# Kernel optimization log

Hardware: AMD Instinct MI355X
Metric: run time of the kernel (lower is better)

## Reference

```python
import jax, jax.numpy as jnp
import numpy as np

B, C, N, V, W = 2, 4, 224, 7, 256
EMB, H = 256, 4
TOKEN_DIM = C * N           # 896
HF = int(C * 2.66)          # 10 (GDFN hidden features)
EPS_LN = 1e-6


def _dwconv3(x, w):
    # depthwise 3x3, padding=1; x:[B,Ch,Hh,Ww], w:[Ch,1,3,3]
    return jax.lax.conv_general_dilated(
        x, w, window_strides=(1, 1), padding='SAME',
        feature_group_count=x.shape[1],
        dimension_numbers=('NCHW', 'OIHW', 'NCHW'))


def _layernorm_c(x, g, b):
    # LayerNorm over channel dim (NCHW), eps=1e-6
    m = jnp.mean(x, axis=1, keepdims=True)
    v = jnp.mean((x - m) ** 2, axis=1, keepdims=True)
    return (x - m) / jnp.sqrt(v + EPS_LN) * g[None, :, None, None] + b[None, :, None, None]


def setup_inputs() -> dict:
    key = jax.random.key(0)
    ks = jax.random.split(key, 12)
    s = 0.02
    return {
        'buffer':     jax.random.normal(ks[0], (B, C, N, V, W), jnp.float32),
        'w_in':       jax.random.normal(ks[1], (EMB, TOKEN_DIM), jnp.float32) * s,
        'temperature': jnp.ones((1, H, 1, 1), jnp.float32),
        'ln1_g':      jnp.ones((EMB,), jnp.float32),
        'ln1_b':      jnp.zeros((EMB,), jnp.float32),
        'w_qkv':      jax.random.normal(ks[2], (3 * EMB, EMB), jnp.float32) * s,
        'w_qkv_dw':   jax.random.normal(ks[3], (3 * EMB, 1, 3, 3), jnp.float32) * s,
        'w_proj':     jax.random.normal(ks[4], (TOKEN_DIM, EMB), jnp.float32) * s,
        'w_attca':    jax.random.normal(ks[5], (2 * H, H), jnp.float32) * s,
        'ln2_g':      jnp.ones((C,), jnp.float32),
        'ln2_b':      jnp.zeros((C,), jnp.float32),
        'w_pin':      jax.random.normal(ks[6], (2 * HF, C), jnp.float32) * s,
        'w_dw':       jax.random.normal(ks[7], (2 * HF, 1, 3, 3), jnp.float32) * s,
        'w_pout':     jax.random.normal(ks[8], (C, HF), jnp.float32) * s,
    }


def reference(buffer, w_in, temperature, ln1_g, ln1_b, w_qkv, w_qkv_dw,
              w_proj, w_attca, ln2_g, ln2_b, w_pin, w_dw, w_pout):
    S = V * W
    d = EMB // H
    # b c n v w -> b (v w) (c n)
    x_tok = buffer.transpose(0, 3, 4, 1, 2).reshape(B, S, C * N)
    # b c n v w -> (b n) c v w
    x_res = buffer.transpose(0, 2, 1, 3, 4).reshape(B * N, C, V, W)

    x_tok = jnp.einsum('bsk,ek->bse', x_tok, w_in)                  # linear_in
    x = x_tok.reshape(B, V, W, EMB).transpose(0, 3, 1, 2)           # b emb v w
    x_norm = _layernorm_c(x, ln1_g, ln1_b)

    qkv = jnp.einsum('bchw,oc->bohw', x_norm, w_qkv)                # 1x1 conv
    qkv = _dwconv3(qkv, w_qkv_dw)
    q, k, v_ = jnp.split(qkv, 3, axis=1)

    def heads(t):  # b (h d) v w -> b h (v w) d
        return t.reshape(B, H, d, S).transpose(0, 1, 3, 2)
    q, k, v_ = heads(q), heads(k), heads(v_)

    # F.normalize(dim=-1), eps=1e-12
    q = q / jnp.maximum(jnp.linalg.norm(q, axis=-1, keepdims=True), 1e-12)
    k = k / jnp.maximum(jnp.linalg.norm(k, axis=-1, keepdims=True), 1e-12)

    attn_logits = jnp.einsum('bhid,bhjd->bhij', q, k) * temperature
    attn0 = jax.nn.softmax(attn_logits, axis=-1)
    attn1 = jnp.maximum(attn_logits, 0.0) ** 2
    attn1 = jax.nn.gelu(attn1, approximate=False) * attn1
    x_att = jnp.einsum('bhij,oh->boij', attn1, w_attca)             # 1x1 conv over heads
    scale, shift = jnp.split(x_att, 2, axis=1)
    attn = attn0 * (1.0 + scale) + shift

    out = jnp.einsum('bhij,bhjd->bhid', attn, v_)
    out = out.transpose(0, 1, 3, 2).reshape(B, EMB, V, W)           # b (h d) v w
    out = jnp.einsum('bchw,oc->bohw', out, w_proj)                  # proj to token_dim
    out = out.reshape(B, C, N, V, W).transpose(0, 2, 1, 3, 4).reshape(B * N, C, V, W)

    x2 = x_res + out
    epi = _layernorm_c(x2, ln2_g, ln2_b)
    # GDFN
    h_ = jnp.einsum('bchw,oc->bohw', epi, w_pin)
    h_ = _dwconv3(h_, w_dw)
    h1, h2 = jnp.split(h_, 2, axis=1)
    h_ = jax.nn.gelu(h1, approximate=False) * h2
    epi = jnp.einsum('bchw,oc->bohw', h_, w_pout)
    epi = x2 + epi

    return epi.reshape(B, N, C, V, W).transpose(0, 2, 1, 3, 4)      # b c n v w
```

## Files before the change

### kernel.cpp

```cpp
#include <hip/hip_runtime.h>
#include <math.h>

#define B_ 2
#define C_ 4
#define N_ 224
#define V_ 7
#define W_ 256
#define S_ 1792
#define EMB_ 256
#define H_ 4
#define D_ 64
#define TOK_ 896
#define HF_ 10
#define JC_ 8
#define JRANGE_ (S_ / JC_)
#define JSTEPS_ (JRANGE_ / 32)

typedef __attribute__((ext_vector_type(8))) short short8;
typedef __attribute__((ext_vector_type(4))) float f32x4;

#define MFMA16(a, b, c) __builtin_amdgcn_mfma_f32_16x16x32_bf16(a, b, c, 0, 0, 0)

__device__ inline short f2bf(float f) {
    union { float f; unsigned u; } x; x.f = f;
    unsigned u = x.u;
    unsigned r = (u + 0x7fffu + ((u >> 16) & 1u)) >> 16;
    return (short)r;
}
__device__ inline float bf2f(short s) {
    union { unsigned u; float f; } x;
    x.u = ((unsigned)(unsigned short)s) << 16;
    return x.f;
}

__global__ __launch_bounds__(256) void gemm64_kernel(
    const float* __restrict__ A, const float* __restrict__ Bact, float* __restrict__ Cm,
    int M, int N, int K, long b_bs, long c_bs,
    const float* __restrict__ mu, const float* __restrict__ ri,
    const float* __restrict__ lg, const float* __restrict__ lb)
{
    const int bz = blockIdx.z;
    Bact += (long)bz * b_bs;
    Cm   += (long)bz * c_bs;
    const int m0 = blockIdx.y * 64, n0 = blockIdx.x * 64;
    __shared__ __align__(16) short As[64 * 32];
    __shared__ __align__(16) short Bs[64 * 32];
    const int t = threadIdx.x;
    const int lane = t & 63, wave = t >> 6;
    const int wr = wave >> 1, wc = wave & 1;
    const int col = lane & 15, grp = lane >> 4;
    const int s_row = t >> 2, s_ch = t & 3;
    const int bn = t & 63, bkc = t >> 6;
    float mun = 0.f, rin = 1.f;
    if (mu) { mun = mu[(long)bz * N + n0 + bn]; rin = ri[(long)bz * N + n0 + bn]; }
    f32x4 acc[2][2];
    #pragma unroll
    for (int i = 0; i < 2; ++i)
        #pragma unroll
        for (int j = 0; j < 2; ++j) acc[i][j] = (f32x4){0.f, 0.f, 0.f, 0.f};
    for (int k0 = 0; k0 < K; k0 += 32) {
        const float* ap = &A[(long)(m0 + s_row) * K + k0 + s_ch * 8];
        f32x4 a0 = *(const f32x4*)ap;
        f32x4 a1 = *(const f32x4*)(ap + 4);
        short8 av;
        av[0] = f2bf(a0[0]); av[1] = f2bf(a0[1]); av[2] = f2bf(a0[2]); av[3] = f2bf(a0[3]);
        av[4] = f2bf(a1[0]); av[5] = f2bf(a1[1]); av[6] = f2bf(a1[2]); av[7] = f2bf(a1[3]);
        int abyte = (s_row << 6) + (s_ch << 4);
        *(short8*)((char*)As + (abyte ^ ((s_row & 7) << 4))) = av;
        short8 bw;
        #pragma unroll
        for (int j = 0; j < 8; ++j) {
            float v = Bact[(long)(k0 + bkc * 8 + j) * N + n0 + bn];
            if (mu) v = fmaf((v - mun) * rin, lg[k0 + bkc * 8 + j], lb[k0 + bkc * 8 + j]);
            bw[j] = f2bf(v);
        }
        int bbyte = (bn << 6) + (bkc << 4);
        *(short8*)((char*)Bs + (bbyte ^ ((bn & 7) << 4))) = bw;
        __syncthreads();
        short8 af[2], bfv[2];
        #pragma unroll
        for (int mm = 0; mm < 2; ++mm) {
            int r = wr * 32 + mm * 16 + col;
            af[mm] = *(const short8*)((const char*)As + ((((r) << 6) + (grp << 4)) ^ ((r & 7) << 4)));
        }
        #pragma unroll
        for (int nn = 0; nn < 2; ++nn) {
            int r = wc * 32 + nn * 16 + col;
            bfv[nn] = *(const short8*)((const char*)Bs + ((((r) << 6) + (grp << 4)) ^ ((r & 7) << 4)));
        }
        #pragma unroll
        for (int mm = 0; mm < 2; ++mm)
            #pragma unroll
            for (int nn = 0; nn < 2; ++nn)
                acc[mm][nn] = MFMA16(af[mm], bfv[nn], acc[mm][nn]);
        __syncthreads();
    }
    #pragma unroll
    for (int mm = 0; mm < 2; ++mm)
        #pragma unroll
        for (int nn = 0; nn < 2; ++nn)
            #pragma unroll
            for (int r = 0; r < 4; ++r)
                Cm[(long)(m0 + wr * 32 + mm * 16 + grp * 4 + r) * N
                   + n0 + wc * 32 + nn * 16 + col] = acc[mm][nn][r];
}

__global__ __launch_bounds__(256) void ln1stats_kernel(
    const float* __restrict__ X, float* __restrict__ mu, float* __restrict__ ri)
{
    int sl = threadIdx.x & 63, dg = threadIdx.x >> 6;
    int s = blockIdx.x * 64 + sl;
    int img = blockIdx.y;
    const float* xp = X + (long)img * EMB_ * S_ + s;
    float sum = 0.f, sq = 0.f;
    for (int c = dg * 64; c < dg * 64 + 64; ++c) {
        float v = xp[(long)c * S_];
        sum += v; sq += v * v;
    }
    __shared__ float rs[64][5], rq[64][5];
    rs[sl][dg] = sum; rq[sl][dg] = sq;
    __syncthreads();
    if (dg == 0) {
        float tot = rs[sl][0] + rs[sl][1] + rs[sl][2] + rs[sl][3];
        float tq  = rq[sl][0] + rq[sl][1] + rq[sl][2] + rq[sl][3];
        float mean = tot * (1.f / EMB_);
        float var  = tq * (1.f / EMB_) - mean * mean;
        mu[(long)img * S_ + s] = mean;
        ri[(long)img * S_ + s] = rsqrtf(var + 1e-6f);
    }
}

__global__ void dwconv3_kernel(const float* __restrict__ X, const float* __restrict__ Wt,
                               float* __restrict__ Y, short* __restrict__ vbf,
                               long total, int Ch)
{
    long idx = (long)blockIdx.x * blockDim.x + threadIdx.x;
    long stride = (long)gridDim.x * blockDim.x;
    for (; idx < total; idx += stride) {
        int w = (int)(idx % W_);
        long t = idx / W_;
        int h = (int)(t % V_); t /= V_;
        int ch = (int)(t % Ch);
        long img_ch = idx / ((long)V_ * W_);
        const float* wp = Wt + ch * 9;
        const float* xp = X + img_ch * (V_ * W_);
        float acc = 0.f;
        #pragma unroll
        for (int dy = -1; dy <= 1; ++dy) {
            int h2 = h + dy;
            if (h2 < 0 || h2 >= V_) continue;
            #pragma unroll
            for (int dx = -1; dx <= 1; ++dx) {
                int w2 = w + dx;
                if (w2 < 0 || w2 >= W_) continue;
                acc += xp[h2 * W_ + w2] * wp[(dy + 1) * 3 + (dx + 1)];
            }
        }
        Y[idx] = acc;
        if (vbf && ch >= 512) {
            int b = (int)(t / Ch);
            vbf[((long)b * 256 + (ch - 512)) * S_ + h * W_ + w] = f2bf(acc);
        }
    }
}

__global__ __launch_bounds__(256) void headnorm_kernel(
    const float* __restrict__ qkvd, const float* __restrict__ temp,
    short* __restrict__ qn, short* __restrict__ kn)
{
    int s0 = blockIdx.x * 64;
    int bh = blockIdx.y; int b = bh >> 2, h = bh & 3;
    int isq = blockIdx.z;
    int ch0 = b * 768 + (isq ? 0 : EMB_) + h * 64;
    short* dst = (isq ? qn : kn) + (long)bh * S_ * 64;
    __shared__ float tile[64][65];
    __shared__ float red[64][4];
    int t = threadIdx.x;
    int sl = t & 63, dg = t >> 6;
    float part = 0.f;
    for (int dd = 0; dd < 16; ++dd) {
        int d = dg * 16 + dd;
        float v = qkvd[(long)(ch0 + d) * S_ + s0 + sl];
        tile[sl][d] = v;
        part += v * v;
    }
    red[sl][dg] = part;
    __syncthreads();
    int d = t & 63, sg = t >> 6;
    float tmul = isq ? temp[h] : 1.f;
    for (int si = 0; si < 16; ++si) {
        int s = sg * 16 + si;
        float nrm = sqrtf(red[s][0] + red[s][1] + red[s][2] + red[s][3]);
        float scale = tmul / fmaxf(nrm, 1e-12f);
        dst[(long)(s0 + s) * 64 + d] = f2bf(tile[s][d] * scale);
    }
}

__global__ __launch_bounds__(256) void attn_kernel(
    const short* __restrict__ qn, const short* __restrict__ kn,
    const short* __restrict__ vbf, const float* __restrict__ wat,
    float* __restrict__ partY, float* __restrict__ partZ)
{
    const int h = threadIdx.x >> 6;
    const int lane = threadIdx.x & 63;
    const int col = lane & 15, grp = lane >> 4;
    const int itile = blockIdx.x;
    const int jc = blockIdx.y;
    const int b = blockIdx.z;
    const int ibase = itile * 16;
    const int bh = b * 4 + h;

    const short* qrow = qn + ((long)bh * S_ + ibase + col) * 64 + grp * 8;
    short8 qa0 = *(const short8*)qrow;
    short8 qa1 = *(const short8*)(qrow + 32);
    float wsc[4], wsh[4];
    #pragma unroll
    for (int hh = 0; hh < 4; ++hh) { wsc[hh] = wat[h * 4 + hh]; wsh[hh] = wat[(4 + h) * 4 + hh]; }

    __shared__ float exch[4][32][34];

    f32x4 y1[4], y2[4];
    #pragma unroll
    for (int dt = 0; dt < 4; ++dt) {
        y1[dt] = (f32x4){0.f, 0.f, 0.f, 0.f};
        y2[dt] = (f32x4){0.f, 0.f, 0.f, 0.f};
    }
    float z = 0.f;
    const short* kbase = kn + (long)bh * S_ * 64;
    const short* vbase = vbf + ((long)b * 256 + h * 64) * S_;
    const int joffA = (col & 3) + 8 * (col >> 2);

    for (int jt = 0; jt < JSTEPS_; ++jt) {
        int jbase = jc * JRANGE_ + jt * 32;
        f32x4 lf[2];
        #pragma unroll
        for (int tt = 0; tt < 2; ++tt) {
            const short* krow = kbase + (long)(jbase + joffA + 4 * tt) * 64 + grp * 8;
            short8 ka0 = *(const short8*)krow;
            short8 ka1 = *(const short8*)(krow + 32);
            f32x4 a = (f32x4){0.f, 0.f, 0.f, 0.f};
            a = MFMA16(ka0, qa0, a);
            a = MFMA16(ka1, qa1, a);
            lf[tt] = a;
        }
        float a1own[2][4], ee[2][4];
        #pragma unroll
        for (int tt = 0; tt < 2; ++tt)
            #pragma unroll
            for (int r = 0; r < 4; ++r) {
                float l = lf[tt][r];
                float rr = fmaxf(l, 0.f);
                float s1 = rr * rr;
                float u = fmaf(s1 * s1, 0.0713548162726f * s1, 1.59576912161f * s1);
                float sg = __builtin_amdgcn_rcpf(1.f + __expf(-u));
                float a1 = s1 * sg * s1;
                a1own[tt][r] = a1;
                ee[tt][r] = __expf(l);
                exch[h][r + 4 * tt + 8 * grp][col] = a1;
            }
        __syncthreads();
        short8 pa, pb;
        #pragma unroll
        for (int tt = 0; tt < 2; ++tt)
            #pragma unroll
            for (int r = 0; r < 4; ++r) {
                int jloc = r + 4 * tt + 8 * grp;
                float sc = 0.f, sh = 0.f;
                #pragma unroll
                for (int hh = 0; hh < 4; ++hh) {
                    float a1v = (hh == h) ? a1own[tt][r] : exch[hh][jloc][col];
                    sc += a1v * wsc[hh];
                    sh += a1v * wsh[hh];
                }
                float e = ee[tt][r];
                z += e;
                pa[tt * 4 + r] = f2bf(e * (1.f + sc));
                pb[tt * 4 + r] = f2bf(sh);
            }
        __syncthreads();
        #pragma unroll
        for (int dt = 0; dt < 4; ++dt) {
            const short* vrow = vbase + (long)(dt * 16 + col) * S_ + jbase + grp * 8;
            short8 vb = *(const short8*)vrow;
            y1[dt] = MFMA16(pa, vb, y1[dt]);
            y2[dt] = MFMA16(pb, vb, y2[dt]);
        }
    }

    z += __shfl_xor(z, 16, 64);
    z += __shfl_xor(z, 32, 64);
    if (grp == 0)
        partZ[((long)(jc * 2 + b) * 4 + h) * S_ + ibase + col] = z;

    __syncthreads();
    float* tb = &exch[h][0][0];
    long ybase = ((((long)jc * 2 + b) * 4 + h) * 2) * 64 * S_;
    for (int acc = 0; acc < 2; ++acc) {
        #pragma unroll
        for (int dt = 0; dt < 4; ++dt) {
            f32x4 y = acc ? y2[dt] : y1[dt];
            #pragma unroll
            for (int r = 0; r < 4; ++r) tb[(grp * 4 + r) * 17 + col] = y[r];
            #pragma unroll
            for (int p = 0; p < 4; ++p) {
                float val = tb[col * 17 + p * 4 + grp];
                partY[ybase + ((long)acc * 64 + dt * 16 + p * 4 + grp) * S_ + ibase + col] = val;
            }
        }
    }
}

__global__ __launch_bounds__(256) void combine_kernel(
    const float* __restrict__ partY, const float* __restrict__ partZ,
    float* __restrict__ outav)
{
    int idx = blockIdx.x * 256 + threadIdx.x;
    int i = idx % S_;
    int t = idx / S_;
    int d = t & 63; t >>= 6;
    int h = t & 3; int b = t >> 2;
    float y1 = 0.f, y2 = 0.f, z = 0.f;
    #pragma unroll
    for (int jc = 0; jc < JC_; ++jc) {
        long base = ((((long)jc * 2 + b) * 4 + h) * 2) * 64 * S_;
        y1 += partY[base + (long)d * S_ + i];
        y2 += partY[base + (long)(64 + d) * S_ + i];
        z  += partZ[((long)(jc * 2 + b) * 4 + h) * S_ + i];
    }
    outav[((long)b * 256 + h * 64 + d) * S_ + i] = y1 / z + y2;
}

__global__ __launch_bounds__(256) void resid_pin_kernel(
    const float* __restrict__ buffer, const float* __restrict__ proj,
    const float* __restrict__ g2, const float* __restrict__ b2,
    const float* __restrict__ w_pin,
    float* __restrict__ x2, short* __restrict__ hbuf)
{
    int s = blockIdx.x * 256 + threadIdx.x;
    int bn = blockIdx.y;
    int b = bn / N_, n = bn % N_;
    float v[4];
    float sum = 0.f;
    #pragma unroll
    for (int c = 0; c < 4; ++c) {
        float xr = buffer[((long)(b * 4 + c) * N_ + n) * S_ + s];
        float pr = proj[((long)b * TOK_ + c * N_ + n) * S_ + s];
        v[c] = xr + pr;
        x2[((long)bn * 4 + c) * S_ + s] = v[c];
        sum += v[c];
    }
    float mean = sum * 0.25f;
    float var = 0.f;
    #pragma unroll
    for (int c = 0; c < 4; ++c) { float dd = v[c] - mean; var += dd * dd; }
    var *= 0.25f;
    float inv = rsqrtf(var + 1e-6f);
    float e[4];
    #pragma unroll
    for (int c = 0; c < 4; ++c) e[c] = (v[c] - mean) * inv * g2[c] + b2[c];
    for (int o = 0; o < 2 * HF_; ++o) {
        float a = 0.f;
        #pragma unroll
        for (int c = 0; c < 4; ++c) a += w_pin[o * 4 + c] * e[c];
        hbuf[((long)bn * (2 * HF_) + o) * S_ + s] = f2bf(a);
    }
}

__global__ __launch_bounds__(448) void gdfn_kernel(
    const short* __restrict__ hbuf, const float* __restrict__ w_dw,
    const float* __restrict__ w_pout, const float* __restrict__ x2,
    float* __restrict__ out)
{
    int xt = blockIdx.x;
    int bn = blockIdx.y;
    int b = bn / N_, n = bn % N_;
    int x0 = xt * 64;
    __shared__ float tile[20][7][66];
    int tid = threadIdx.x;
    for (int idx = tid; idx < 20 * 7 * 66; idx += 448) {
        int ch = idx / (7 * 66); int rem = idx % (7 * 66);
        int y = rem / 66; int xx = rem % 66;
        int gx = x0 + xx - 1;
        float v = 0.f;
        if (gx >= 0 && gx < W_) v = bf2f(hbuf[((long)bn * 20 + ch) * S_ + y * W_ + gx]);
        tile[ch][y][xx] = v;
    }
    __syncthreads();
    int y = tid / 64, x = tid & 63;
    float hd[20];
    #pragma unroll
    for (int ch = 0; ch < 20; ++ch) {
        const float* wp = w_dw + ch * 9;
        float acc = 0.f;
        #pragma unroll
        for (int dy = -1; dy <= 1; ++dy) {
            int yy = y + dy;
            if (yy < 0 || yy >= V_) continue;
            #pragma unroll
            for (int dx = -1; dx <= 1; ++dx)
                acc += tile[ch][yy][x + 1 + dx] * wp[(dy + 1) * 3 + (dx + 1)];
        }
        hd[ch] = acc;
    }
    float g[HF_];
    #pragma unroll
    for (int f = 0; f < HF_; ++f) {
        float h1 = hd[f];
        g[f] = 0.5f * h1 * (1.f + erff(h1 * 0.70710678118654752f)) * hd[HF_ + f];
    }
    int s = y * W_ + x0 + x;
    #pragma unroll
    for (int c = 0; c < 4; ++c) {
        float a = 0.f;
        #pragma unroll
        for (int f = 0; f < HF_; ++f) a += w_pout[c * HF_ + f] * g[f];
        out[((long)(b * 4 + c) * N_ + n) * S_ + s] = x2[((long)bn * 4 + c) * S_ + s] + a;
    }
}

extern "C" void kernel_launch(void* const* d_in, const int* in_sizes, int n_in,
                              void* d_out, int out_size, void* d_ws, size_t ws_size,
                              hipStream_t stream)
{
    const float* buffer = (const float*)d_in[0];
    const float* w_in   = (const float*)d_in[1];
    const float* temp   = (const float*)d_in[2];
    const float* ln1_g  = (const float*)d_in[3];
    const float* ln1_b  = (const float*)d_in[4];
    const float* w_qkv  = (const float*)d_in[5];
    const float* w_qkv_dw = (const float*)d_in[6];
    const float* w_proj = (const float*)d_in[7];
    const float* w_attca = (const float*)d_in[8];
    const float* ln2_g  = (const float*)d_in[9];
    const float* ln2_b  = (const float*)d_in[10];
    const float* w_pin  = (const float*)d_in[11];
    const float* w_dw   = (const float*)d_in[12];
    const float* w_pout = (const float*)d_in[13];
    float* out = (float*)d_out;

    float* ws = (float*)d_ws;
    float* qkvd    = ws;
    short* qn      = (short*)(ws + 2752512);
    short* kn      = (short*)(ws + 3211264);
    short* vbf     = (short*)(ws + 3670016);
    float* partY   = ws + 4128768;
    float* partZ   = ws + 18808832;
    float* outav   = ws + 18923520;
    float* xw      = ws + 19841024;
    float* mu      = ws + 20758528;
    float* ri      = ws + 20762112;
    float* qkv     = ws + 20765696;
    float* outproj = ws + 23518208;
    float* x2      = ws + 26729472;
    short* hbuf    = (short*)(ws + 29940736);

    gemm64_kernel<<<dim3(28, 4, 2), 256, 0, stream>>>(
        w_in, buffer, xw, EMB_, S_, TOK_, (long)TOK_ * S_, (long)EMB_ * S_,
        nullptr, nullptr, nullptr, nullptr);

    ln1stats_kernel<<<dim3(28, 2), 256, 0, stream>>>(xw, mu, ri);

    gemm64_kernel<<<dim3(28, 12, 2), 256, 0, stream>>>(
        w_qkv, xw, qkv, 3 * EMB_, S_, EMB_, (long)EMB_ * S_, (long)3 * EMB_ * S_,
        mu, ri, ln1_g, ln1_b);

    {
        long total = (long)B_ * 3 * EMB_ * S_;
        dwconv3_kernel<<<(int)((total + 255) / 256), 256, 0, stream>>>(
            qkv, w_qkv_dw, qkvd, vbf, total, 3 * EMB_);
    }

    headnorm_kernel<<<dim3(28, 8, 2), 256, 0, stream>>>(qkvd, temp, qn, kn);

    attn_kernel<<<dim3(112, JC_, B_), 256, 0, stream>>>(qn, kn, vbf, w_attca, partY, partZ);

    combine_kernel<<<3584, 256, 0, stream>>>(partY, partZ, outav);

    gemm64_kernel<<<dim3(28, 14, 2), 256, 0, stream>>>(
        w_proj, outav, outproj, TOK_, S_, EMB_, (long)EMB_ * S_, (long)TOK_ * S_,
        nullptr, nullptr, nullptr, nullptr);

    resid_pin_kernel<<<dim3(7, B_ * N_), 256, 0, stream>>>(
        buffer, outproj, ln2_g, ln2_b, w_pin, x2, hbuf);

    gdfn_kernel<<<dim3(4, B_ * N_), 448, 0, stream>>>(hbuf, w_dw, w_pout, x2, out);
}
```

Before: 237.2 us.

## Fuse LN1 stats into GEMM epilogue, widen GEMM tiles, bf16 attention partials

Templates the GEMM to a 64x128 tile and computes per-column sum and sum-of-squares in the epilogue of the first GEMM, so the separate LN1 stats kernel goes away and the next GEMM derives mean and rstd from the partial column sums. The attention split over j goes from 8 chunks to 4, partial Y and outav are stored as bf16 to cut memory traffic, and the head-mixing exchange uses double-buffered vectorized LDS with one fewer barrier and s_setprio hints. The projection GEMM reads bf16 input directly. The costs are fewer blocks in several launches, lower precision in the partial sums, and variance computed from summed partials.

```diff
diff --git a/kernel.cpp b/kernel.cpp
--- a/kernel.cpp
+++ b/kernel.cpp
@@ -12,7 +12,7 @@
 #define D_ 64
 #define TOK_ 896
 #define HF_ 10
-#define JC_ 8
+#define JC_ 4
 #define JRANGE_ (S_ / JC_)
 #define JSTEPS_ (JRANGE_ / 32)
 
@@ -33,100 +33,128 @@
     return x.f;
 }
 
-__global__ __launch_bounds__(256) void gemm64_kernel(
-    const float* __restrict__ A, const float* __restrict__ Bact, float* __restrict__ Cm,
+template<bool COLSUM, bool LNB, bool BBF>
+__global__ __launch_bounds__(256) void gemm_kernel(
+    const float* __restrict__ A, const void* __restrict__ Bv, float* __restrict__ Cm,
     int M, int N, int K, long b_bs, long c_bs,
-    const float* __restrict__ mu, const float* __restrict__ ri,
+    const float* __restrict__ csin, float* __restrict__ csout,
     const float* __restrict__ lg, const float* __restrict__ lb)
 {
     const int bz = blockIdx.z;
-    Bact += (long)bz * b_bs;
-    Cm   += (long)bz * c_bs;
-    const int m0 = blockIdx.y * 64, n0 = blockIdx.x * 64;
+    Cm += (long)bz * c_bs;
+    const int m0 = blockIdx.y * 64, n0 = blockIdx.x * 128;
     __shared__ __align__(16) short As[64 * 32];
-    __shared__ __align__(16) short Bs[64 * 32];
+    __shared__ __align__(16) short Bs[128 * 32];
     const int t = threadIdx.x;
     const int lane = t & 63, wave = t >> 6;
     const int wr = wave >> 1, wc = wave & 1;
     const int col = lane & 15, grp = lane >> 4;
-    const int s_row = t >> 2, s_ch = t & 3;
-    const int bn = t & 63, bkc = t >> 6;
-    float mun = 0.f, rin = 1.f;
-    if (mu) { mun = mu[(long)bz * N + n0 + bn]; rin = ri[(long)bz * N + n0 + bn]; }
-    f32x4 acc[2][2];
+    const int arow = t >> 2, akc = (t & 3) * 8;
+    const int bn = t & 127, bkc = (t >> 7) * 16;
+    float mean = 0.f, rstd = 1.f;
+    if (LNB) {
+        float s = 0.f, q = 0.f;
+        #pragma unroll
+        for (int mb = 0; mb < 4; ++mb) {
+            s += csin[((long)(bz * 4 + mb) * 2 + 0) * N + n0 + bn];
+            q += csin[((long)(bz * 4 + mb) * 2 + 1) * N + n0 + bn];
+        }
+        mean = s * (1.f / 256.f);
+        rstd = rsqrtf(q * (1.f / 256.f) - mean * mean + 1e-6f);
+    }
+    f32x4 acc[2][4];
     #pragma unroll
     for (int i = 0; i < 2; ++i)
         #pragma unroll
-        for (int j = 0; j < 2; ++j) acc[i][j] = (f32x4){0.f, 0.f, 0.f, 0.f};
+        for (int j = 0; j < 4; ++j) acc[i][j] = (f32x4){0.f, 0.f, 0.f, 0.f};
     for (int k0 = 0; k0 < K; k0 += 32) {
-        const float* ap = &A[(long)(m0 + s_row) * K + k0 + s_ch * 8];
-        f32x4 a0 = *(const f32x4*)ap;
-        f32x4 a1 = *(const f32x4*)(ap + 4);
-        short8 av;
-        av[0] = f2bf(a0[0]); av[1] = f2bf(a0[1]); av[2] = f2bf(a0[2]); av[3] = f2bf(a0[3]);
-        av[4] = f2bf(a1[0]); av[5] = f2bf(a1[1]); av[6] = f2bf(a1[2]); av[7] = f2bf(a1[3]);
-        int abyte = (s_row << 6) + (s_ch << 4);
-        *(short8*)((char*)As + (abyte ^ ((s_row & 7) << 4))) = av;
-        short8 bw;
-        #pragma unroll
-        for (int j = 0; j < 8; ++j) {
-            float v = Bact[(long)(k0 + bkc * 8 + j) * N + n0 + bn];
-            if (mu) v = fmaf((v - mun) * rin, lg[k0 + bkc * 8 + j], lb[k0 + bkc * 8 + j]);
-            bw[j] = f2bf(v);
-        }
-        int bbyte = (bn << 6) + (bkc << 4);
-        *(short8*)((char*)Bs + (bbyte ^ ((bn & 7) << 4))) = bw;
+        {
+            const float* ap = &A[(long)(m0 + arow) * K + k0 + akc];
+            f32x4 a0 = *(const f32x4*)ap;
+            f32x4 a1 = *(const f32x4*)(ap + 4);
+            short8 av;
+            av[0] = f2bf(a0[0]); av[1] = f2bf(a0[1]); av[2] = f2bf(a0[2]); av[3] = f2bf(a0[3]);
+            av[4] = f2bf(a1[0]); av[5] = f2bf(a1[1]); av[6] = f2bf(a1[2]); av[7] = f2bf(a1[3]);
+            int abyte = (arow << 6) + (akc << 1);
+            *(short8*)((char*)As + (abyte ^ ((arow & 7) << 4))) = av;
+        }
+        {
+            short8 b0, b1;
+            if (BBF) {
+                const short* Bp = (const short*)Bv + (long)bz * b_bs;
+                #pragma unroll
+                for (int j = 0; j < 8; ++j) {
+                    b0[j] = Bp[(long)(k0 + bkc + j) * N + n0 + bn];
+                    b1[j] = Bp[(long)(k0 + bkc + 8 + j) * N + n0 + bn];
+                }
+            } else {
+                const float* Bp = (const float*)Bv + (long)bz * b_bs;
+                #pragma unroll
+                for (int j = 0; j < 16; ++j) {
+                    float v = Bp[(long)(k0 + bkc + j) * N + n0 + bn];
+                    if (LNB) v = fmaf((v - mean) * rstd, lg[k0 + bkc + j], lb[k0 + bkc + j]);
+                    if (j < 8) b0[j] = f2bf(v); else b1[j - 8] = f2bf(v);
+                }
+            }
+            int bbyte = (bn << 6) + (bkc << 1);
+            *(short8*)((char*)Bs + ((bbyte) ^ ((bn & 7) << 4))) = b0;
+            *(short8*)((char*)Bs + ((bbyte + 16) ^ ((bn & 7) << 4))) = b1;
+        }
         __syncthreads();
-        short8 af[2], bfv[2];
+        short8 af[2], bfv[4];
         #pragma unroll
         for (int mm = 0; mm < 2; ++mm) {
             int r = wr * 32 + mm * 16 + col;
-            af[mm] = *(const short8*)((const char*)As + ((((r) << 6) + (grp << 4)) ^ ((r & 7) << 4)));
-        }
-        #pragma unroll
-        for (int nn = 0; nn < 2; ++nn) {
-            int r = wc * 32 + nn * 16 + col;
-            bfv[nn] = *(const short8*)((const char*)Bs + ((((r) << 6) + (grp << 4)) ^ ((r & 7) << 4)));
+            af[mm] = *(const short8*)((const char*)As + (((r << 6) + (grp << 4)) ^ ((r & 7) << 4)));
+        }
+        #pragma unroll
+        for (int nn = 0; nn < 4; ++nn) {
+            int r = wc * 64 + nn * 16 + col;
+            bfv[nn] = *(const short8*)((const char*)Bs + (((r << 6) + (grp << 4)) ^ ((r & 7) << 4)));
         }
         #pragma unroll
         for (int mm = 0; mm < 2; ++mm)
             #pragma unroll
-            for (int nn = 0; nn < 2; ++nn)
+            for (int nn = 0; nn < 4; ++nn)
                 acc[mm][nn] = MFMA16(af[mm], bfv[nn], acc[mm][nn]);
         __syncthreads();
     }
     #pragma unroll
     for (int mm = 0; mm < 2; ++mm)
         #pragma unroll
-        for (int nn = 0; nn < 2; ++nn)
+        for (int nn = 0; nn < 4; ++nn)
             #pragma unroll
             for (int r = 0; r < 4; ++r)
                 Cm[(long)(m0 + wr * 32 + mm * 16 + grp * 4 + r) * N
-                   + n0 + wc * 32 + nn * 16 + col] = acc[mm][nn][r];
-}
-
-__global__ __launch_bounds__(256) void ln1stats_kernel(
-    const float* __restrict__ X, float* __restrict__ mu, float* __restrict__ ri)
-{
-    int sl = threadIdx.x & 63, dg = threadIdx.x >> 6;
-    int s = blockIdx.x * 64 + sl;
-    int img = blockIdx.y;
-    const float* xp = X + (long)img * EMB_ * S_ + s;
-    float sum = 0.f, sq = 0.f;
-    for (int c = dg * 64; c < dg * 64 + 64; ++c) {
-        float v = xp[(long)c * S_];
-        sum += v; sq += v * v;
-    }
-    __shared__ float rs[64][5], rq[64][5];
-    rs[sl][dg] = sum; rq[sl][dg] = sq;
-    __syncthreads();
-    if (dg == 0) {
-        float tot = rs[sl][0] + rs[sl][1] + rs[sl][2] + rs[sl][3];
-        float tq  = rq[sl][0] + rq[sl][1] + rq[sl][2] + rq[sl][3];
-        float mean = tot * (1.f / EMB_);
-        float var  = tq * (1.f / EMB_) - mean * mean;
-        mu[(long)img * S_ + s] = mean;
-        ri[(long)img * S_ + s] = rsqrtf(var + 1e-6f);
+                   + n0 + wc * 64 + nn * 16 + col] = acc[mm][nn][r];
+    if (COLSUM) {
+        float* red = (float*)As;
+        #pragma unroll
+        for (int nn = 0; nn < 4; ++nn) {
+            float s = 0.f, q = 0.f;
+            #pragma unroll
+            for (int mm = 0; mm < 2; ++mm)
+                #pragma unroll
+                for (int r = 0; r < 4; ++r) { float v = acc[mm][nn][r]; s += v; q += v * v; }
+            s += __shfl_xor(s, 16, 64); s += __shfl_xor(s, 32, 64);
+            q += __shfl_xor(q, 16, 64); q += __shfl_xor(q, 32, 64);
+            if (lane < 16) {
+                int cidx = wc * 64 + nn * 16 + col;
+                red[(wr * 128 + cidx) * 2]     = s;
+                red[(wr * 128 + cidx) * 2 + 1] = q;
+            }
+        }
+        __syncthreads();
+        if (wave < 2 && lane < 16) {
+            #pragma unroll
+            for (int nn = 0; nn < 4; ++nn) {
+                int cidx = wc * 64 + nn * 16 + col;
+                float s = red[cidx * 2]     + red[(128 + cidx) * 2];
+                float q = red[cidx * 2 + 1] + red[(128 + cidx) * 2 + 1];
+                csout[((long)(bz * 4 + blockIdx.y) * 2 + 0) * N + n0 + cidx] = s;
+                csout[((long)(bz * 4 + blockIdx.y) * 2 + 1) * N + n0 + cidx] = q;
+            }
+        }
     }
 }
 
@@ -199,7 +227,7 @@
 __global__ __launch_bounds__(256) void attn_kernel(
     const short* __restrict__ qn, const short* __restrict__ kn,
     const short* __restrict__ vbf, const float* __restrict__ wat,
-    float* __restrict__ partY, float* __restrict__ partZ)
+    short* __restrict__ partY, float* __restrict__ partZ)
 {
     const int h = threadIdx.x >> 6;
     const int lane = threadIdx.x & 63;
@@ -217,7 +245,7 @@
     #pragma unroll
     for (int hh = 0; hh < 4; ++hh) { wsc[hh] = wat[h * 4 + hh]; wsh[hh] = wat[(4 + h) * 4 + hh]; }
 
-    __shared__ float exch[4][32][34];
+    __shared__ __align__(16) float exch[2][4][16][36];
 
     f32x4 y1[4], y2[4];
     #pragma unroll
@@ -231,8 +259,10 @@
     const int joffA = (col & 3) + 8 * (col >> 2);
 
     for (int jt = 0; jt < JSTEPS_; ++jt) {
-        int jbase = jc * JRANGE_ + jt * 32;
+        const int jbase = jc * JRANGE_ + jt * 32;
+        const int buf = jt & 1;
         f32x4 lf[2];
+        __builtin_amdgcn_s_setprio(1);
         #pragma unroll
         for (int tt = 0; tt < 2; ++tt) {
             const short* krow = kbase + (long)(jbase + joffA + 4 * tt) * 64 + grp * 8;
@@ -243,9 +273,11 @@
             a = MFMA16(ka1, qa1, a);
             lf[tt] = a;
         }
-        float a1own[2][4], ee[2][4];
-        #pragma unroll
-        for (int tt = 0; tt < 2; ++tt)
+        __builtin_amdgcn_s_setprio(0);
+        f32x4 a1v[2];
+        float ee[2][4];
+        #pragma unroll
+        for (int tt = 0; tt < 2; ++tt) {
             #pragma unroll
             for (int r = 0; r < 4; ++r) {
                 float l = lf[tt][r];
@@ -253,31 +285,33 @@
                 float s1 = rr * rr;
                 float u = fmaf(s1 * s1, 0.0713548162726f * s1, 1.59576912161f * s1);
                 float sg = __builtin_amdgcn_rcpf(1.f + __expf(-u));
-                float a1 = s1 * sg * s1;
-                a1own[tt][r] = a1;
+                a1v[tt][r] = s1 * sg * s1;
                 ee[tt][r] = __expf(l);
-                exch[h][r + 4 * tt + 8 * grp][col] = a1;
-            }
+            }
+            *(f32x4*)&exch[buf][h][col][8 * grp + 4 * tt] = a1v[tt];
+        }
         __syncthreads();
         short8 pa, pb;
         #pragma unroll
-        for (int tt = 0; tt < 2; ++tt)
+        for (int tt = 0; tt < 2; ++tt) {
+            f32x4 scv = a1v[tt] * wsc[h];
+            f32x4 shv = a1v[tt] * wsh[h];
+            #pragma unroll
+            for (int hh = 0; hh < 4; ++hh) {
+                if (hh == h) continue;
+                f32x4 o = *(const f32x4*)&exch[buf][hh][col][8 * grp + 4 * tt];
+                scv += o * wsc[hh];
+                shv += o * wsh[hh];
+            }
             #pragma unroll
             for (int r = 0; r < 4; ++r) {
-                int jloc = r + 4 * tt + 8 * grp;
-                float sc = 0.f, sh = 0.f;
-                #pragma unroll
-                for (int hh = 0; hh < 4; ++hh) {
-                    float a1v = (hh == h) ? a1own[tt][r] : exch[hh][jloc][col];
-                    sc += a1v * wsc[hh];
-                    sh += a1v * wsh[hh];
-                }
                 float e = ee[tt][r];
                 z += e;
-                pa[tt * 4 + r] = f2bf(e * (1.f + sc));
-                pb[tt * 4 + r] = f2bf(sh);
-            }
-        __syncthreads();
+                pa[tt * 4 + r] = f2bf(e * (1.f + scv[r]));
+                pb[tt * 4 + r] = f2bf(shv[r]);
+            }
+        }
+        __builtin_amdgcn_s_setprio(1);
         #pragma unroll
         for (int dt = 0; dt < 4; ++dt) {
             const short* vrow = vbase + (long)(dt * 16 + col) * S_ + jbase + grp * 8;
@@ -285,6 +319,7 @@
             y1[dt] = MFMA16(pa, vb, y1[dt]);
             y2[dt] = MFMA16(pb, vb, y2[dt]);
         }
+        __builtin_amdgcn_s_setprio(0);
     }
 
     z += __shfl_xor(z, 16, 64);
@@ -292,8 +327,7 @@
     if (grp == 0)
         partZ[((long)(jc * 2 + b) * 4 + h) * S_ + ibase + col] = z;
 
-    __syncthreads();
-    float* tb = &exch[h][0][0];
+    float* tb = &exch[0][h][0][0];
     long ybase = ((((long)jc * 2 + b) * 4 + h) * 2) * 64 * S_;
     for (int acc = 0; acc < 2; ++acc) {
         #pragma unroll
@@ -304,15 +338,15 @@
             #pragma unroll
             for (int p = 0; p < 4; ++p) {
                 float val = tb[col * 17 + p * 4 + grp];
-                partY[ybase + ((long)acc * 64 + dt * 16 + p * 4 + grp) * S_ + ibase + col] = val;
+                partY[ybase + ((long)acc * 64 + dt * 16 + p * 4 + grp) * S_ + ibase + col] = f2bf(val);
             }
         }
     }
 }
 
 __global__ __launch_bounds__(256) void combine_kernel(
-    const float* __restrict__ partY, const float* __restrict__ partZ,
-    float* __restrict__ outav)
+    const short* __restrict__ partY, const float* __restrict__ partZ,
+    short* __restrict__ outav)
 {
     int idx = blockIdx.x * 256 + threadIdx.x;
     int i = idx % S_;
@@ -323,11 +357,11 @@
     #pragma unroll
     for (int jc = 0; jc < JC_; ++jc) {
         long base = ((((long)jc * 2 + b) * 4 + h) * 2) * 64 * S_;
-        y1 += partY[base + (long)d * S_ + i];
-        y2 += partY[base + (long)(64 + d) * S_ + i];
+        y1 += bf2f(partY[base + (long)d * S_ + i]);
+        y2 += bf2f(partY[base + (long)(64 + d) * S_ + i]);
         z  += partZ[((long)(jc * 2 + b) * 4 + h) * S_ + i];
     }
-    outav[((long)b * 256 + h * 64 + d) * S_ + i] = y1 / z + y2;
+    outav[((long)b * 256 + h * 64 + d) * S_ + i] = f2bf(y1 / z + y2);
 }
 
 __global__ __launch_bounds__(256) void resid_pin_kernel(
@@ -443,26 +477,23 @@
     short* qn      = (short*)(ws + 2752512);
     short* kn      = (short*)(ws + 3211264);
     short* vbf     = (short*)(ws + 3670016);
-    float* partY   = ws + 4128768;
-    float* partZ   = ws + 18808832;
-    float* outav   = ws + 18923520;
-    float* xw      = ws + 19841024;
-    float* mu      = ws + 20758528;
-    float* ri      = ws + 20762112;
-    float* qkv     = ws + 20765696;
-    float* outproj = ws + 23518208;
-    float* x2      = ws + 26729472;
-    short* hbuf    = (short*)(ws + 29940736);
-
-    gemm64_kernel<<<dim3(28, 4, 2), 256, 0, stream>>>(
+    short* partY   = (short*)(ws + 4128768);
+    float* partZ   = ws + 7798784;
+    short* outav   = (short*)(ws + 7856128);
+    float* xw      = ws + 8314880;
+    float* colsum  = ws + 9232384;
+    float* qkv     = ws + 9261056;
+    float* outproj = ws + 12013568;
+    float* x2      = ws + 15224832;
+    short* hbuf    = (short*)(ws + 18436096);
+
+    gemm_kernel<true, false, false><<<dim3(14, 4, 2), 256, 0, stream>>>(
         w_in, buffer, xw, EMB_, S_, TOK_, (long)TOK_ * S_, (long)EMB_ * S_,
-        nullptr, nullptr, nullptr, nullptr);
-
-    ln1stats_kernel<<<dim3(28, 2), 256, 0, stream>>>(xw, mu, ri);
-
-    gemm64_kernel<<<dim3(28, 12, 2), 256, 0, stream>>>(
+        nullptr, colsum, nullptr, nullptr);
+
+    gemm_kernel<false, true, false><<<dim3(14, 12, 2), 256, 0, stream>>>(
         w_qkv, xw, qkv, 3 * EMB_, S_, EMB_, (long)EMB_ * S_, (long)3 * EMB_ * S_,
-        mu, ri, ln1_g, ln1_b);
+        colsum, nullptr, ln1_g, ln1_b);
 
     {
         long total = (long)B_ * 3 * EMB_ * S_;
@@ -476,7 +507,7 @@
 
     combine_kernel<<<3584, 256, 0, stream>>>(partY, partZ, outav);
 
-    gemm64_kernel<<<dim3(28, 14, 2), 256, 0, stream>>>(
+    gemm_kernel<false, false, true><<<dim3(14, 14, 2), 256, 0, stream>>>(
         w_proj, outav, outproj, TOK_, S_, EMB_, (long)EMB_ * S_, (long)TOK_ * S_,
         nullptr, nullptr, nullptr, nullptr);
 
```

Result: faster. 217.2 us (-8.4%).
